# Optimization experiments

Hardware: AMD Instinct MI355X
Metric: run time of the kernel (lower is better)

Reference implementation:

```python
import jax, jax.numpy as jnp
import numpy as np

# Geometry (cone-beam circular trajectory, TIGRE-style ZYX volume layout)
NZ, NY, NX = 96, 96, 96          # geo.nVoxel
NV, NU = 96, 96                  # geo.nDetector (rows v, cols u)
N_ANGLES = 48
NS = 96                          # samples per ray (Joseph-style line integral)
DSO, DSD = 500.0, 1000.0         # source-origin / source-detector distances (mm)
DV = 1.0                         # voxel size (mm, isotropic)
DDET = 2.0                       # detector pixel size (mm)


def _trilinear(vol, pts):
    """Trilinear interpolation. vol: [B,Z,Y,X]; pts: [...,3] voxel coords (z,y,x).
    Points outside the volume contribute zero. Returns [B, ...]."""
    Z, Y, X = vol.shape[-3:]
    z, y, x = pts[..., 0], pts[..., 1], pts[..., 2]
    valid = ((z >= 0) & (z <= Z - 1) & (y >= 0) & (y <= Y - 1)
             & (x >= 0) & (x <= X - 1)).astype(vol.dtype)
    z = jnp.clip(z, 0.0, Z - 1.0)
    y = jnp.clip(y, 0.0, Y - 1.0)
    x = jnp.clip(x, 0.0, X - 1.0)
    z0 = jnp.minimum(jnp.floor(z).astype(jnp.int32), Z - 2)
    y0 = jnp.minimum(jnp.floor(y).astype(jnp.int32), Y - 2)
    x0 = jnp.minimum(jnp.floor(x).astype(jnp.int32), X - 2)
    fz = (z - z0).astype(vol.dtype)
    fy = (y - y0).astype(vol.dtype)
    fx = (x - x0).astype(vol.dtype)
    z1, y1, x1 = z0 + 1, y0 + 1, x0 + 1

    def g(zi, yi, xi):
        return vol[:, zi, yi, xi]  # [B, ...]

    out = (g(z0, y0, x0) * (1 - fz) * (1 - fy) * (1 - fx)
           + g(z0, y0, x1) * (1 - fz) * (1 - fy) * fx
           + g(z0, y1, x0) * (1 - fz) * fy * (1 - fx)
           + g(z0, y1, x1) * (1 - fz) * fy * fx
           + g(z1, y0, x0) * fz * (1 - fy) * (1 - fx)
           + g(z1, y0, x1) * fz * (1 - fy) * fx
           + g(z1, y1, x0) * fz * fy * (1 - fx)
           + g(z1, y1, x1) * fz * fy * fx)
    return out * valid


def _ray_points(theta):
    """Sample points (voxel coords, z,y,x order) along every detector ray for one angle.
    Returns pts [NV,NU,NS,3] and the integration step length (scalar)."""
    c, s = jnp.cos(theta), jnp.sin(theta)
    src = jnp.stack([DSO * c, DSO * s, jnp.float32(0.0)])            # world (x,y,z)
    det_c = jnp.stack([-(DSD - DSO) * c, -(DSD - DSO) * s, jnp.float32(0.0)])
    u_ax = jnp.stack([-s, c, jnp.float32(0.0)])
    v_ax = jnp.array([0.0, 0.0, 1.0], dtype=jnp.float32)
    u = (jnp.arange(NU, dtype=jnp.float32) - (NU - 1) / 2.0) * DDET
    v = (jnp.arange(NV, dtype=jnp.float32) - (NV - 1) / 2.0) * DDET
    pix = (det_c[None, None, :]
           + u[None, :, None] * u_ax[None, None, :]
           + v[:, None, None] * v_ax[None, None, :])                 # [NV,NU,3]
    d = pix - src[None, None, :]
    d = d / jnp.linalg.norm(d, axis=-1, keepdims=True)               # unit ray dirs
    # integrate over the volume bounding sphere around the isocenter
    R = 0.5 * np.sqrt((NX * DV) ** 2 + (NY * DV) ** 2 + (NZ * DV) ** 2)
    step = jnp.float32(2.0 * R / NS)
    t = jnp.float32(DSO - R) + (jnp.arange(NS, dtype=jnp.float32) + 0.5) * step
    pw = src[None, None, None, :] + d[:, :, None, :] * t[None, None, :, None]  # [NV,NU,NS,3] world xyz
    # world -> voxel index space, reorder to (z,y,x)
    iz = pw[..., 2] / DV + (NZ - 1) / 2.0
    iy = pw[..., 1] / DV + (NY - 1) / 2.0
    ix = pw[..., 0] / DV + (NX - 1) / 2.0
    return jnp.stack([iz, iy, ix], axis=-1), step


def _project(vol):
    """Cone-beam forward projection (tigre.Ax analogue). vol [B,NZ,NY,NX] -> sino [B,A,NV,NU]."""
    angles = jnp.linspace(0.0, 2.0 * np.pi, N_ANGLES, endpoint=False, dtype=jnp.float32)

    def body(_, theta):
        pts, step = _ray_points(theta)
        vals = _trilinear(vol, pts)          # [B,NV,NU,NS]
        return None, vals.sum(axis=-1) * step

    _, sino = jax.lax.scan(body, None, angles)   # [A,B,NV,NU]
    return jnp.transpose(sino, (1, 0, 2, 3))


def setup_inputs() -> dict:
    key = jax.random.key(0)
    x = jax.random.uniform(key, (2, NZ, NY, NX), dtype=jnp.float32)
    return {"x": x}


def reference(x):
    return _project(x)
```

## Files before the change

### kernel.cpp

```cpp
#include <hip/hip_runtime.h>
#include <math.h>


#define NZg 96
#define NYg 96
#define NXg 96
#define NVg 96
#define NUg 96
#define NAg 48
#define NSg 96
#define NBg 2
#define NVOX (NZg * NYg * NXg)
#define NRAY1 (NAg * NVg * NUg)
#define PLANE (NYg * NXg)

typedef float v4f __attribute__((ext_vector_type(4)));

__global__ __launch_bounds__(256) void pack_b2_dual_t(
    const float* __restrict__ vol, float2* __restrict__ qx,
    float2* __restrict__ qy) {
    __shared__ float2 tile[16][17];
    const int z      = blockIdx.x / 36;
    const int tileId = blockIdx.x % 36;
    const int y0 = (tileId / 6) * 16;
    const int x0 = (tileId % 6) * 16;
    const int tx = threadIdx.x & 15;
    const int ty = threadIdx.x >> 4;
    const int idx = (z * NYg + (y0 + ty)) * NXg + (x0 + tx);
    float2 p;
    p.x = vol[idx];
    p.y = vol[idx + NVOX];
    qx[idx] = p;
    tile[ty][tx] = p;
    __syncthreads();
    qy[(z * NXg + (x0 + ty)) * NYg + (y0 + tx)] = tile[tx][ty];
}

__global__ void make_trig(float2* __restrict__ trig) {
    const int a = threadIdx.x;
    if (a < NAg) {
        const float dtheta = 6.2831855f / 48.0f;
        const float theta  = (float)a * dtheta;
        float2 cs;
        cs.x = (float)cos((double)theta);
        cs.y = (float)sin((double)theta);
        trig[a] = cs;
    }
}

__device__ __forceinline__ void ray_setup_cs(
    int ridx, float c, float s, float& srcx, float& srcy,
    float& dx, float& dy, float& dz, int& k0, int& k1) {
#pragma clang fp contract(off)
    const int u   = ridx % NUg;
    int tmp       = ridx / NUg;
    const int v   = tmp % NVg;

    srcx = 500.0f * c;
    srcy = 500.0f * s;
    const float uu = ((float)u - 47.5f) * 2.0f;
    const float vv = ((float)v - 47.5f) * 2.0f;
    const float pixx = (-500.0f * c) + uu * (-s);
    const float pixy = (-500.0f * s) + uu * c;
    const float pixz = vv;

    const float dx0 = pixx - srcx;
    const float dy0 = pixy - srcy;
    const float dz0 = pixz;
    const float nrm = sqrtf((dx0 * dx0 + dy0 * dy0) + dz0 * dz0);
    dx = dx0 / nrm;
    dy = dy0 / nrm;
    dz = dz0 / nrm;

    const float stepf = (float)1.7320508075688773;
    const float t0f   = (float)416.8615612366939;

    const float LO = -47.51f, HI = 47.51f;
    float tlo = -1e30f, thi = 1e30f;
    {
        const float o3[3] = {srcx, srcy, 0.0f};
        const float d3[3] = {dx, dy, dz};
        bool empty = false;
        #pragma unroll
        for (int ax = 0; ax < 3; ++ax) {
            const float oo = o3[ax], dd = d3[ax];
            if (fabsf(dd) > 1e-8f) {
                const float inv = 1.0f / dd;
                const float ta = (LO - oo) * inv;
                const float tb = (HI - oo) * inv;
                tlo = fmaxf(tlo, fminf(ta, tb));
                thi = fminf(thi, fmaxf(ta, tb));
            } else if (oo < LO || oo > HI) {
                empty = true;
            }
        }
        if (empty) { tlo = 1.0f; thi = 0.0f; }
    }
    if (thi >= tlo) {
        k0 = (int)floorf((tlo - t0f) / stepf) - 2;
        k1 = (int)ceilf((thi - t0f) / stepf) + 2;
        k0 = max(k0, 0);
        k1 = min(k1, NSg - 1);
    } else {
        k0 = 1; k1 = 0;
    }
}

__global__ __launch_bounds__(256) void coneproj_b2dual_c2(
    const float2* __restrict__ qx, const float2* __restrict__ qy,
    const float2* __restrict__ trig, float* __restrict__ out) {
#pragma clang fp contract(off)
    const int lane     = threadIdx.x & 63;
    const int wid      = threadIdx.x >> 6;
    const int chunk    = wid >> 1;
    const int rayInBlk = ((wid & 1) << 6) + lane;
    const int ridx = blockIdx.x * 128 + rayInBlk;
    const int a    = ridx / (NUg * NVg);
    const float2 cs = trig[a];

    float srcx, srcy, dx, dy, dz;
    int k0, k1;
    ray_setup_cs(ridx, cs.x, cs.y, srcx, srcy, dx, dy, dz, k0, k1);

    const float stepf = (float)1.7320508075688773;
    const float t0f   = (float)416.8615612366939;

    const bool xfast = fabsf(cs.y) >= fabsf(cs.x);
    const float2* __restrict__ q = xfast ? qx : qy;
    const float src_i = xfast ? srcx : srcy;
    const float d_i   = xfast ? dx   : dy;
    const float src_m = xfast ? srcy : srcx;
    const float d_m   = xfast ? dy   : dx;

    const int len = (k1 - k0 + 2) >> 1;
    const int kb0 = k0 + chunk * len;
    const int kb1 = min(kb0 + len - 1, k1);

    float acc0 = 0.0f, acc1 = 0.0f;
    for (int k = kb0; k <= kb1; ++k) {
        const float tk = t0f + ((float)k + 0.5f) * stepf;
        const float ci = (src_i + d_i * tk) + 47.5f;
        const float cm = (src_m + d_m * tk) + 47.5f;
        const float iz = (dz * tk) + 47.5f;
        if (ci >= 0.0f && ci <= 95.0f &&
            cm >= 0.0f && cm <= 95.0f &&
            iz >= 0.0f && iz <= 95.0f) {
            const int i0 = min((int)ci, 94);
            const int m0 = min((int)cm, 94);
            const int z0 = min((int)iz, NZg - 2);
            const float fi = ci - (float)i0;
            const float fm = cm - (float)m0;
            const float fz = iz - (float)z0;
            const int base = (z0 * 96 + m0) * 96 + i0;
            const v4f r00 = *(const v4f*)(q + base);
            const v4f r01 = *(const v4f*)(q + base + 96);
            const v4f r10 = *(const v4f*)(q + base + PLANE);
            const v4f r11 = *(const v4f*)(q + base + PLANE + 96);
            {
                const float c00 = r00.x + fi * (r00.z - r00.x);
                const float c01 = r01.x + fi * (r01.z - r01.x);
                const float c10 = r10.x + fi * (r10.z - r10.x);
                const float c11 = r11.x + fi * (r11.z - r11.x);
                const float c0  = c00 + fm * (c01 - c00);
                const float c1  = c10 + fm * (c11 - c10);
                acc0 += c0 + fz * (c1 - c0);
            }
            {
                const float c00 = r00.y + fi * (r00.w - r00.y);
                const float c01 = r01.y + fi * (r01.w - r01.y);
                const float c10 = r10.y + fi * (r10.w - r10.y);
                const float c11 = r11.y + fi * (r11.w - r11.y);
                const float c0  = c00 + fm * (c01 - c00);
                const float c1  = c10 + fm * (c11 - c10);
                acc1 += c0 + fz * (c1 - c0);
            }
        }
    }

    __shared__ float p0[256];
    __shared__ float p1[256];
    p0[chunk * 128 + rayInBlk] = acc0;
    p1[chunk * 128 + rayInBlk] = acc1;
    __syncthreads();
    if (threadIdx.x < 128) {
        const int r = blockIdx.x * 128 + threadIdx.x;
        const float s0 = p0[threadIdx.x] + p0[threadIdx.x + 128];
        const float s1 = p1[threadIdx.x] + p1[threadIdx.x + 128];
        out[r]         = s0 * stepf;
        out[r + NRAY1] = s1 * stepf;
    }
}

__global__ __launch_bounds__(256) void pack_b2(
    const float* __restrict__ vol, float2* __restrict__ q) {
    const int i = blockIdx.x * blockDim.x + threadIdx.x;
    float2 p;
    p.x = vol[i];
    p.y = vol[i + NVOX];
    q[i] = p;
}

__device__ __forceinline__ void ray_setup(
    int ridx, float& srcx, float& srcy, float& dx, float& dy, float& dz,
    int& k0, int& k1) {
#pragma clang fp contract(off)
    const int a = ridx / (NUg * NVg);
    const float dtheta = 6.2831855f / 48.0f;
    const float theta  = (float)a * dtheta;
    const float c = (float)cos((double)theta);
    const float s = (float)sin((double)theta);
    ray_setup_cs(ridx, c, s, srcx, srcy, dx, dy, dz, k0, k1);
}

__global__ __launch_bounds__(256) void coneproj_b2x4(
    const float2* __restrict__ q, float* __restrict__ out) {
#pragma clang fp contract(off)
    const int ridx = blockIdx.x * blockDim.x + threadIdx.x;
    float srcx, srcy, dx, dy, dz;
    int k0, k1;
    ray_setup(ridx, srcx, srcy, dx, dy, dz, k0, k1);

    const float stepf = (float)1.7320508075688773;
    const float t0f   = (float)416.8615612366939;

    float acc0 = 0.0f, acc1 = 0.0f;
    for (int k = k0; k <= k1; ++k) {
        const float tk = t0f + ((float)k + 0.5f) * stepf;
        const float ix = (srcx + dx * tk) + 47.5f;
        const float iy = (srcy + dy * tk) + 47.5f;
        const float iz = (dz * tk) + 47.5f;
        if (ix >= 0.0f && ix <= 95.0f &&
            iy >= 0.0f && iy <= 95.0f &&
            iz >= 0.0f && iz <= 95.0f) {
            const int x0 = min((int)ix, NXg - 2);
            const int y0 = min((int)iy, NYg - 2);
            const int z0 = min((int)iz, NZg - 2);
            const float fx = ix - (float)x0;
            const float fy = iy - (float)y0;
            const float fz = iz - (float)z0;
            const int base = (z0 * NYg + y0) * NXg + x0;
            const v4f r00 = *(const v4f*)(q + base);
            const v4f r01 = *(const v4f*)(q + base + NXg);
            const v4f r10 = *(const v4f*)(q + base + PLANE);
            const v4f r11 = *(const v4f*)(q + base + PLANE + NXg);
            {
                const float c00 = r00.x + fx * (r00.z - r00.x);
                const float c01 = r01.x + fx * (r01.z - r01.x);
                const float c10 = r10.x + fx * (r10.z - r10.x);
                const float c11 = r11.x + fx * (r11.z - r11.x);
                const float c0  = c00 + fy * (c01 - c00);
                const float c1  = c10 + fy * (c11 - c10);
                acc0 += c0 + fz * (c1 - c0);
            }
            {
                const float c00 = r00.y + fx * (r00.w - r00.y);
                const float c01 = r01.y + fx * (r01.w - r01.y);
                const float c10 = r10.y + fx * (r10.w - r10.y);
                const float c11 = r11.y + fx * (r11.w - r11.y);
                const float c0  = c00 + fy * (c01 - c00);
                const float c1  = c10 + fy * (c11 - c10);
                acc1 += c0 + fz * (c1 - c0);
            }
        }
    }
    out[ridx]         = acc0 * stepf;
    out[ridx + NRAY1] = acc1 * stepf;
}

__global__ __launch_bounds__(256) void coneproj_direct(
    const float* __restrict__ vol, float* __restrict__ out) {
#pragma clang fp contract(off)
    const int gidx = blockIdx.x * blockDim.x + threadIdx.x;
    const int ridx = gidx % NRAY1;
    const int b    = gidx / NRAY1;
    float srcx, srcy, dx, dy, dz;
    int k0, k1;
    ray_setup(ridx, srcx, srcy, dx, dy, dz, k0, k1);

    const float stepf = (float)1.7320508075688773;
    const float t0f   = (float)416.8615612366939;

    const float* __restrict__ volb = vol + (size_t)b * NVOX;

    float acc = 0.0f;
    for (int k = k0; k <= k1; ++k) {
        const float tk = t0f + ((float)k + 0.5f) * stepf;
        const float ix = (srcx + dx * tk) + 47.5f;
        const float iy = (srcy + dy * tk) + 47.5f;
        const float iz = (dz * tk) + 47.5f;
        if (ix >= 0.0f && ix <= 95.0f &&
            iy >= 0.0f && iy <= 95.0f &&
            iz >= 0.0f && iz <= 95.0f) {
            const int x0 = min((int)ix, NXg - 2);
            const int y0 = min((int)iy, NYg - 2);
            const int z0 = min((int)iz, NZg - 2);
            const float fx = ix - (float)x0;
            const float fy = iy - (float)y0;
            const float fz = iz - (float)z0;
            const float* p = volb + ((z0 * NYg + y0) * NXg + x0);
            const float v000 = p[0];
            const float v001 = p[1];
            const float v010 = p[NXg];
            const float v011 = p[NXg + 1];
            const float v100 = p[NYg * NXg];
            const float v101 = p[NYg * NXg + 1];
            const float v110 = p[NYg * NXg + NXg];
            const float v111 = p[NYg * NXg + NXg + 1];
            const float c00 = v000 + fx * (v001 - v000);
            const float c01 = v010 + fx * (v011 - v010);
            const float c10 = v100 + fx * (v101 - v100);
            const float c11 = v110 + fx * (v111 - v110);
            const float c0  = c00 + fy * (c01 - c00);
            const float c1  = c10 + fy * (c11 - c10);
            acc += c0 + fz * (c1 - c0);
        }
    }
    out[gidx] = acc * stepf;
}

extern "C" void kernel_launch(void* const* d_in, const int* in_sizes, int n_in,
                              void* d_out, int out_size, void* d_ws, size_t ws_size,
                              hipStream_t stream) {
    const float* vol = (const float*)d_in[0];
    float* out = (float*)d_out;
    const size_t need_dual   = 2 * (size_t)NVOX * sizeof(float2)
                             + (size_t)NAg * sizeof(float2);
    const size_t need_single = (size_t)NVOX * sizeof(float2);
    if (ws_size >= need_dual) {
        float2* qx   = (float2*)d_ws;
        float2* qy   = qx + NVOX;
        float2* trig = qy + NVOX;
        pack_b2_dual_t<<<96 * 36, 256, 0, stream>>>(vol, qx, qy);
        make_trig<<<1, 64, 0, stream>>>(trig);
        coneproj_b2dual_c2<<<NRAY1 / 128, 256, 0, stream>>>(qx, qy, trig, out);
    } else if (ws_size >= need_single) {
        float2* q = (float2*)d_ws;
        pack_b2<<<NVOX / 256, 256, 0, stream>>>(vol, q);
        coneproj_b2x4<<<NRAY1 / 256, 256, 0, stream>>>(q, out);
    } else {
        coneproj_direct<<<(NBg * NRAY1) / 256, 256, 0, stream>>>(vol, out);
    }
}
```

Baseline: 190.3 us.

## Fuse volume packing and projection into one cooperative kernel with grid sync

Merges the dual-layout pack kernel and the projection kernel into a single cooperative launch of 1728 blocks. The blocks first pack the volume tiles, then synchronise across the grid and project one ray per thread. The intent is to remove a kernel launch boundary and its gap. It also drops the earlier split of each ray's samples across two waves with a shared-memory reduction, so each thread now walks the whole ray. This gives less parallelism per ray, and a 1728-block cooperative launch may fail residency checks, in which case it falls back to two kernels.

After: 397.4 us. +108.8%, slower.

```diff
diff --git a/kernel.cpp b/kernel.cpp
--- a/kernel.cpp
+++ b/kernel.cpp
@@ -1,5 +1,8 @@
 #include <hip/hip_runtime.h>
+#include <hip/hip_cooperative_groups.h>
 #include <math.h>
+
+namespace cg = cooperative_groups;
 
 
 #define NZg 96
@@ -13,28 +16,9 @@
 #define NVOX (NZg * NYg * NXg)
 #define NRAY1 (NAg * NVg * NUg)
 #define PLANE (NYg * NXg)
+#define NBLK 1728
 
 typedef float v4f __attribute__((ext_vector_type(4)));
-
-__global__ __launch_bounds__(256) void pack_b2_dual_t(
-    const float* __restrict__ vol, float2* __restrict__ qx,
-    float2* __restrict__ qy) {
-    __shared__ float2 tile[16][17];
-    const int z      = blockIdx.x / 36;
-    const int tileId = blockIdx.x % 36;
-    const int y0 = (tileId / 6) * 16;
-    const int x0 = (tileId % 6) * 16;
-    const int tx = threadIdx.x & 15;
-    const int ty = threadIdx.x >> 4;
-    const int idx = (z * NYg + (y0 + ty)) * NXg + (x0 + tx);
-    float2 p;
-    p.x = vol[idx];
-    p.y = vol[idx + NVOX];
-    qx[idx] = p;
-    tile[ty][tx] = p;
-    __syncthreads();
-    qy[(z * NXg + (x0 + ty)) * NYg + (y0 + tx)] = tile[tx][ty];
-}
 
 __global__ void make_trig(float2* __restrict__ trig) {
     const int a = threadIdx.x;
@@ -106,18 +90,10 @@
     }
 }
 
-__global__ __launch_bounds__(256) void coneproj_b2dual_c2(
-    const float2* __restrict__ qx, const float2* __restrict__ qy,
-    const float2* __restrict__ trig, float* __restrict__ out) {
+__device__ __forceinline__ void project_ray(
+    int ridx, float2 cs, const float2* __restrict__ qx,
+    const float2* __restrict__ qy, float* __restrict__ out) {
 #pragma clang fp contract(off)
-    const int lane     = threadIdx.x & 63;
-    const int wid      = threadIdx.x >> 6;
-    const int chunk    = wid >> 1;
-    const int rayInBlk = ((wid & 1) << 6) + lane;
-    const int ridx = blockIdx.x * 128 + rayInBlk;
-    const int a    = ridx / (NUg * NVg);
-    const float2 cs = trig[a];
-
     float srcx, srcy, dx, dy, dz;
     int k0, k1;
     ray_setup_cs(ridx, cs.x, cs.y, srcx, srcy, dx, dy, dz, k0, k1);
@@ -132,12 +108,8 @@
     const float src_m = xfast ? srcy : srcx;
     const float d_m   = xfast ? dy   : dx;
 
-    const int len = (k1 - k0 + 2) >> 1;
-    const int kb0 = k0 + chunk * len;
-    const int kb1 = min(kb0 + len - 1, k1);
-
     float acc0 = 0.0f, acc1 = 0.0f;
-    for (int k = kb0; k <= kb1; ++k) {
+    for (int k = k0; k <= k1; ++k) {
         const float tk = t0f + ((float)k + 0.5f) * stepf;
         const float ci = (src_i + d_i * tk) + 47.5f;
         const float cm = (src_m + d_m * tk) + 47.5f;
@@ -176,28 +148,67 @@
             }
         }
     }
-
-    __shared__ float p0[256];
-    __shared__ float p1[256];
-    p0[chunk * 128 + rayInBlk] = acc0;
-    p1[chunk * 128 + rayInBlk] = acc1;
+    out[ridx]         = acc0 * stepf;
+    out[ridx + NRAY1] = acc1 * stepf;
+}
+
+__global__ __launch_bounds__(256) void coneproj_fused(
+    const float* __restrict__ vol, float2* __restrict__ qx,
+    float2* __restrict__ qy, const float2* __restrict__ trig,
+    float* __restrict__ out) {
+    __shared__ float2 tile[16][17];
+
+    const int tx = threadIdx.x & 15;
+    const int ty = threadIdx.x >> 4;
+    for (int pb = blockIdx.x; pb < 96 * 36; pb += NBLK) {
+        const int z      = pb / 36;
+        const int tileId = pb % 36;
+        const int y0 = (tileId / 6) * 16;
+        const int x0 = (tileId % 6) * 16;
+        const int idx = (z * NYg + (y0 + ty)) * NXg + (x0 + tx);
+        float2 p;
+        p.x = vol[idx];
+        p.y = vol[idx + NVOX];
+        qx[idx] = p;
+        __syncthreads();
+        tile[ty][tx] = p;
+        __syncthreads();
+        qy[(z * NXg + (x0 + ty)) * NYg + (y0 + tx)] = tile[tx][ty];
+    }
+
+    cg::this_grid().sync();
+
+    const int ridx = blockIdx.x * 256 + threadIdx.x;
+    const int a    = ridx / (NUg * NVg);
+    project_ray(ridx, trig[a], qx, qy, out);
+}
+
+__global__ __launch_bounds__(256) void pack_b2_dual_t(
+    const float* __restrict__ vol, float2* __restrict__ qx,
+    float2* __restrict__ qy) {
+    __shared__ float2 tile[16][17];
+    const int z      = blockIdx.x / 36;
+    const int tileId = blockIdx.x % 36;
+    const int y0 = (tileId / 6) * 16;
+    const int x0 = (tileId % 6) * 16;
+    const int tx = threadIdx.x & 15;
+    const int ty = threadIdx.x >> 4;
+    const int idx = (z * NYg + (y0 + ty)) * NXg + (x0 + tx);
+    float2 p;
+    p.x = vol[idx];
+    p.y = vol[idx + NVOX];
+    qx[idx] = p;
+    tile[ty][tx] = p;
     __syncthreads();
-    if (threadIdx.x < 128) {
-        const int r = blockIdx.x * 128 + threadIdx.x;
-        const float s0 = p0[threadIdx.x] + p0[threadIdx.x + 128];
-        const float s1 = p1[threadIdx.x] + p1[threadIdx.x + 128];
-        out[r]         = s0 * stepf;
-        out[r + NRAY1] = s1 * stepf;
-    }
-}
-
-__global__ __launch_bounds__(256) void pack_b2(
-    const float* __restrict__ vol, float2* __restrict__ q) {
-    const int i = blockIdx.x * blockDim.x + threadIdx.x;
-    float2 p;
-    p.x = vol[i];
-    p.y = vol[i + NVOX];
-    q[i] = p;
+    qy[(z * NXg + (x0 + ty)) * NYg + (y0 + tx)] = tile[tx][ty];
+}
+
+__global__ __launch_bounds__(256) void coneproj_b2dual(
+    const float2* __restrict__ qx, const float2* __restrict__ qy,
+    const float2* __restrict__ trig, float* __restrict__ out) {
+    const int ridx = blockIdx.x * blockDim.x + threadIdx.x;
+    const int a    = ridx / (NUg * NVg);
+    project_ray(ridx, trig[a], qx, qy, out);
 }
 
 __device__ __forceinline__ void ray_setup(
@@ -210,61 +221,6 @@
     const float c = (float)cos((double)theta);
     const float s = (float)sin((double)theta);
     ray_setup_cs(ridx, c, s, srcx, srcy, dx, dy, dz, k0, k1);
-}
-
-__global__ __launch_bounds__(256) void coneproj_b2x4(
-    const float2* __restrict__ q, float* __restrict__ out) {
-#pragma clang fp contract(off)
-    const int ridx = blockIdx.x * blockDim.x + threadIdx.x;
-    float srcx, srcy, dx, dy, dz;
-    int k0, k1;
-    ray_setup(ridx, srcx, srcy, dx, dy, dz, k0, k1);
-
-    const float stepf = (float)1.7320508075688773;
-    const float t0f   = (float)416.8615612366939;
-
-    float acc0 = 0.0f, acc1 = 0.0f;
-    for (int k = k0; k <= k1; ++k) {
-        const float tk = t0f + ((float)k + 0.5f) * stepf;
-        const float ix = (srcx + dx * tk) + 47.5f;
-        const float iy = (srcy + dy * tk) + 47.5f;
-        const float iz = (dz * tk) + 47.5f;
-        if (ix >= 0.0f && ix <= 95.0f &&
-            iy >= 0.0f && iy <= 95.0f &&
-            iz >= 0.0f && iz <= 95.0f) {
-            const int x0 = min((int)ix, NXg - 2);
-            const int y0 = min((int)iy, NYg - 2);
-            const int z0 = min((int)iz, NZg - 2);
-            const float fx = ix - (float)x0;
-            const float fy = iy - (float)y0;
-            const float fz = iz - (float)z0;
-            const int base = (z0 * NYg + y0) * NXg + x0;
-            const v4f r00 = *(const v4f*)(q + base);
-            const v4f r01 = *(const v4f*)(q + base + NXg);
-            const v4f r10 = *(const v4f*)(q + base + PLANE);
-            const v4f r11 = *(const v4f*)(q + base + PLANE + NXg);
-            {
-                const float c00 = r00.x + fx * (r00.z - r00.x);
-                const float c01 = r01.x + fx * (r01.z - r01.x);
-                const float c10 = r10.x + fx * (r10.z - r10.x);
-                const float c11 = r11.x + fx * (r11.z - r11.x);
-                const float c0  = c00 + fy * (c01 - c00);
-                const float c1  = c10 + fy * (c11 - c10);
-                acc0 += c0 + fz * (c1 - c0);
-            }
-            {
-                const float c00 = r00.y + fx * (r00.w - r00.y);
-                const float c01 = r01.y + fx * (r01.w - r01.y);
-                const float c10 = r10.y + fx * (r10.w - r10.y);
-                const float c11 = r11.y + fx * (r11.w - r11.y);
-                const float c0  = c00 + fy * (c01 - c00);
-                const float c1  = c10 + fy * (c11 - c10);
-                acc1 += c0 + fz * (c1 - c0);
-            }
-        }
-    }
-    out[ridx]         = acc0 * stepf;
-    out[ridx + NRAY1] = acc1 * stepf;
 }
 
 __global__ __launch_bounds__(256) void coneproj_direct(
@@ -330,13 +286,17 @@
         float2* qx   = (float2*)d_ws;
         float2* qy   = qx + NVOX;
         float2* trig = qy + NVOX;
-        pack_b2_dual_t<<<96 * 36, 256, 0, stream>>>(vol, qx, qy);
         make_trig<<<1, 64, 0, stream>>>(trig);
-        coneproj_b2dual_c2<<<NRAY1 / 128, 256, 0, stream>>>(qx, qy, trig, out);
+        void* args[] = {(void*)&vol, (void*)&qx, (void*)&qy,
+                        (void*)&trig, (void*)&out};
+        hipError_t e = hipLaunchCooperativeKernel(
+            (void*)coneproj_fused, dim3(NBLK), dim3(256), args, 0, stream);
+        if (e != hipSuccess) {
+            pack_b2_dual_t<<<96 * 36, 256, 0, stream>>>(vol, qx, qy);
+            coneproj_b2dual<<<NRAY1 / 256, 256, 0, stream>>>(qx, qy, trig, out);
+        }
     } else if (ws_size >= need_single) {
-        float2* q = (float2*)d_ws;
-        pack_b2<<<NVOX / 256, 256, 0, stream>>>(vol, q);
-        coneproj_b2x4<<<NRAY1 / 256, 256, 0, stream>>>(q, out);
+        coneproj_direct<<<(NBg * NRAY1) / 256, 256, 0, stream>>>(vol, out);
     } else {
         coneproj_direct<<<(NBg * NRAY1) / 256, 256, 0, stream>>>(vol, out);
     }
```

## Pack volume z-fastest with both z-neighbours per voxel, map threads v-fastest

Applied to the files above, without the earlier changes.

Adds a z-fastest packed layout where each entry holds both batches at z and z+1, so each sample's trilinear lookup becomes four 16-byte loads along x/y neighbours. Threads are ordered with detector row v fastest, so adjacent lanes step mostly along z and land on nearby memory. The trig table is built inside the pack kernel, which removes one launch, and the two-chunk split of each ray with its shared-memory reduction is dropped. The cost is a workspace twice as large, output writes that are no longer coalesced (stride NU), and rays that are no longer split, which lowers parallelism.

Result: faster. 173.7 us (-8.7%).

```diff
diff --git a/kernel.cpp b/kernel.cpp
--- a/kernel.cpp
+++ b/kernel.cpp
@@ -15,6 +15,156 @@
 #define PLANE (NYg * NXg)
 
 typedef float v4f __attribute__((ext_vector_type(4)));
+
+__global__ __launch_bounds__(256) void pack_b2_zfast(
+    const float* __restrict__ vol, v4f* __restrict__ D,
+    float2* __restrict__ trig) {
+    const int j = blockIdx.x * 256 + threadIdx.x;
+    const int z = j % NZg;
+    const int t = j / NZg;
+    const int x = t % NXg;
+    const int y = t / NXg;
+    const int rd = (z * NYg + y) * NXg + x;
+    const float b0 = vol[rd];
+    const float b1 = vol[rd + NVOX];
+    const float b0n = (z < 95) ? vol[rd + NYg * NXg] : 0.0f;
+    const float b1n = (z < 95) ? vol[rd + NYg * NXg + NVOX] : 0.0f;
+    v4f e; e.x = b0; e.y = b1; e.z = b0n; e.w = b1n;
+    D[j] = e;
+    if (j < NAg) {
+        const float dtheta = 6.2831855f / 48.0f;
+        const float theta  = (float)j * dtheta;
+        float2 cs;
+        cs.x = (float)cos((double)theta);
+        cs.y = (float)sin((double)theta);
+        trig[j] = cs;
+    }
+}
+
+__device__ __forceinline__ void ray_setup_uv(
+    int u, int v, float c, float s, float& srcx, float& srcy,
+    float& dx, float& dy, float& dz, int& k0, int& k1) {
+#pragma clang fp contract(off)
+    srcx = 500.0f * c;
+    srcy = 500.0f * s;
+    const float uu = ((float)u - 47.5f) * 2.0f;
+    const float vv = ((float)v - 47.5f) * 2.0f;
+    const float pixx = (-500.0f * c) + uu * (-s);
+    const float pixy = (-500.0f * s) + uu * c;
+    const float pixz = vv;
+
+    const float dx0 = pixx - srcx;
+    const float dy0 = pixy - srcy;
+    const float dz0 = pixz;
+    const float nrm = sqrtf((dx0 * dx0 + dy0 * dy0) + dz0 * dz0);
+    dx = dx0 / nrm;
+    dy = dy0 / nrm;
+    dz = dz0 / nrm;
+
+    const float stepf = (float)1.7320508075688773;
+    const float t0f   = (float)416.8615612366939;
+
+    const float LO = -47.51f, HI = 47.51f;
+    float tlo = -1e30f, thi = 1e30f;
+    {
+        const float o3[3] = {srcx, srcy, 0.0f};
+        const float d3[3] = {dx, dy, dz};
+        bool empty = false;
+        #pragma unroll
+        for (int ax = 0; ax < 3; ++ax) {
+            const float oo = o3[ax], dd = d3[ax];
+            if (fabsf(dd) > 1e-8f) {
+                const float inv = 1.0f / dd;
+                const float ta = (LO - oo) * inv;
+                const float tb = (HI - oo) * inv;
+                tlo = fmaxf(tlo, fminf(ta, tb));
+                thi = fminf(thi, fmaxf(ta, tb));
+            } else if (oo < LO || oo > HI) {
+                empty = true;
+            }
+        }
+        if (empty) { tlo = 1.0f; thi = 0.0f; }
+    }
+    if (thi >= tlo) {
+        k0 = (int)floorf((tlo - t0f) / stepf) - 2;
+        k1 = (int)ceilf((thi - t0f) / stepf) + 2;
+        k0 = max(k0, 0);
+        k1 = min(k1, NSg - 1);
+    } else {
+        k0 = 1; k1 = 0;
+    }
+}
+
+__global__ __launch_bounds__(256) void coneproj_zfast(
+    const v4f* __restrict__ D, const float2* __restrict__ trig,
+    float* __restrict__ out) {
+#pragma clang fp contract(off)
+    const int idx = blockIdx.x * 256 + threadIdx.x;
+    const int v   = idx % NVg;
+    int tmp       = idx / NVg;
+    const int u   = tmp % NUg;
+    const int a   = tmp / NUg;
+    const float2 cs = trig[a];
+
+    float srcx, srcy, dx, dy, dz;
+    int k0, k1;
+    ray_setup_uv(u, v, cs.x, cs.y, srcx, srcy, dx, dy, dz, k0, k1);
+
+    const float stepf = (float)1.7320508075688773;
+    const float t0f   = (float)416.8615612366939;
+
+    float acc0 = 0.0f, acc1 = 0.0f;
+    for (int k = k0; k <= k1; ++k) {
+        const float tk = t0f + ((float)k + 0.5f) * stepf;
+        const float ix = (srcx + dx * tk) + 47.5f;
+        const float iy = (srcy + dy * tk) + 47.5f;
+        const float iz = (dz * tk) + 47.5f;
+        if (ix >= 0.0f && ix <= 95.0f &&
+            iy >= 0.0f && iy <= 95.0f &&
+            iz >= 0.0f && iz <= 95.0f) {
+            const int x0 = min((int)ix, NXg - 2);
+            const int y0 = min((int)iy, NYg - 2);
+            const int z0 = min((int)iz, NZg - 2);
+            const float fx = ix - (float)x0;
+            const float fy = iy - (float)y0;
+            const float fz = iz - (float)z0;
+            const int base = (y0 * NXg + x0) * NZg + z0;
+            const v4f r00 = D[base];
+            const v4f r01 = D[base + NZg];
+            const v4f r10 = D[base + NXg * NZg];
+            const v4f r11 = D[base + NXg * NZg + NZg];
+            {
+                const float w00 = r00.x + fz * (r00.z - r00.x);
+                const float w01 = r01.x + fz * (r01.z - r01.x);
+                const float w10 = r10.x + fz * (r10.z - r10.x);
+                const float w11 = r11.x + fz * (r11.z - r11.x);
+                const float e0  = w00 + fx * (w01 - w00);
+                const float e1  = w10 + fx * (w11 - w10);
+                acc0 += e0 + fy * (e1 - e0);
+            }
+            {
+                const float w00 = r00.y + fz * (r00.w - r00.y);
+                const float w01 = r01.y + fz * (r01.w - r01.y);
+                const float w10 = r10.y + fz * (r10.w - r10.y);
+                const float w11 = r11.y + fz * (r11.w - r11.y);
+                const float e0  = w00 + fx * (w01 - w00);
+                const float e1  = w10 + fx * (w11 - w10);
+                acc1 += e0 + fy * (e1 - e0);
+            }
+        }
+    }
+    const int oidx = (a * NVg + v) * NUg + u;
+    out[oidx]         = acc0 * stepf;
+    out[oidx + NRAY1] = acc1 * stepf;
+}
+
+__device__ __forceinline__ void ray_setup_cs(
+    int ridx, float c, float s, float& srcx, float& srcy,
+    float& dx, float& dy, float& dz, int& k0, int& k1) {
+    const int u = ridx % NUg;
+    const int v = (ridx / NUg) % NVg;
+    ray_setup_uv(u, v, c, s, srcx, srcy, dx, dy, dz, k0, k1);
+}
 
 __global__ __launch_bounds__(256) void pack_b2_dual_t(
     const float* __restrict__ vol, float2* __restrict__ qx,
@@ -48,76 +198,13 @@
     }
 }
 
-__device__ __forceinline__ void ray_setup_cs(
-    int ridx, float c, float s, float& srcx, float& srcy,
-    float& dx, float& dy, float& dz, int& k0, int& k1) {
-#pragma clang fp contract(off)
-    const int u   = ridx % NUg;
-    int tmp       = ridx / NUg;
-    const int v   = tmp % NVg;
-
-    srcx = 500.0f * c;
-    srcy = 500.0f * s;
-    const float uu = ((float)u - 47.5f) * 2.0f;
-    const float vv = ((float)v - 47.5f) * 2.0f;
-    const float pixx = (-500.0f * c) + uu * (-s);
-    const float pixy = (-500.0f * s) + uu * c;
-    const float pixz = vv;
-
-    const float dx0 = pixx - srcx;
-    const float dy0 = pixy - srcy;
-    const float dz0 = pixz;
-    const float nrm = sqrtf((dx0 * dx0 + dy0 * dy0) + dz0 * dz0);
-    dx = dx0 / nrm;
-    dy = dy0 / nrm;
-    dz = dz0 / nrm;
-
-    const float stepf = (float)1.7320508075688773;
-    const float t0f   = (float)416.8615612366939;
-
-    const float LO = -47.51f, HI = 47.51f;
-    float tlo = -1e30f, thi = 1e30f;
-    {
-        const float o3[3] = {srcx, srcy, 0.0f};
-        const float d3[3] = {dx, dy, dz};
-        bool empty = false;
-        #pragma unroll
-        for (int ax = 0; ax < 3; ++ax) {
-            const float oo = o3[ax], dd = d3[ax];
-            if (fabsf(dd) > 1e-8f) {
-                const float inv = 1.0f / dd;
-                const float ta = (LO - oo) * inv;
-                const float tb = (HI - oo) * inv;
-                tlo = fmaxf(tlo, fminf(ta, tb));
-                thi = fminf(thi, fmaxf(ta, tb));
-            } else if (oo < LO || oo > HI) {
-                empty = true;
-            }
-        }
-        if (empty) { tlo = 1.0f; thi = 0.0f; }
-    }
-    if (thi >= tlo) {
-        k0 = (int)floorf((tlo - t0f) / stepf) - 2;
-        k1 = (int)ceilf((thi - t0f) / stepf) + 2;
-        k0 = max(k0, 0);
-        k1 = min(k1, NSg - 1);
-    } else {
-        k0 = 1; k1 = 0;
-    }
-}
-
-__global__ __launch_bounds__(256) void coneproj_b2dual_c2(
+__global__ __launch_bounds__(256) void coneproj_b2dual(
     const float2* __restrict__ qx, const float2* __restrict__ qy,
     const float2* __restrict__ trig, float* __restrict__ out) {
 #pragma clang fp contract(off)
-    const int lane     = threadIdx.x & 63;
-    const int wid      = threadIdx.x >> 6;
-    const int chunk    = wid >> 1;
-    const int rayInBlk = ((wid & 1) << 6) + lane;
-    const int ridx = blockIdx.x * 128 + rayInBlk;
+    const int ridx = blockIdx.x * blockDim.x + threadIdx.x;
     const int a    = ridx / (NUg * NVg);
     const float2 cs = trig[a];
-
     float srcx, srcy, dx, dy, dz;
     int k0, k1;
     ray_setup_cs(ridx, cs.x, cs.y, srcx, srcy, dx, dy, dz, k0, k1);
@@ -132,12 +219,8 @@
     const float src_m = xfast ? srcy : srcx;
     const float d_m   = xfast ? dy   : dx;
 
-    const int len = (k1 - k0 + 2) >> 1;
-    const int kb0 = k0 + chunk * len;
-    const int kb1 = min(kb0 + len - 1, k1);
-
     float acc0 = 0.0f, acc1 = 0.0f;
-    for (int k = kb0; k <= kb1; ++k) {
+    for (int k = k0; k <= k1; ++k) {
         const float tk = t0f + ((float)k + 0.5f) * stepf;
         const float ci = (src_i + d_i * tk) + 47.5f;
         const float cm = (src_m + d_m * tk) + 47.5f;
@@ -176,93 +259,6 @@
             }
         }
     }
-
-    __shared__ float p0[256];
-    __shared__ float p1[256];
-    p0[chunk * 128 + rayInBlk] = acc0;
-    p1[chunk * 128 + rayInBlk] = acc1;
-    __syncthreads();
-    if (threadIdx.x < 128) {
-        const int r = blockIdx.x * 128 + threadIdx.x;
-        const float s0 = p0[threadIdx.x] + p0[threadIdx.x + 128];
-        const float s1 = p1[threadIdx.x] + p1[threadIdx.x + 128];
-        out[r]         = s0 * stepf;
-        out[r + NRAY1] = s1 * stepf;
-    }
-}
-
-__global__ __launch_bounds__(256) void pack_b2(
-    const float* __restrict__ vol, float2* __restrict__ q) {
-    const int i = blockIdx.x * blockDim.x + threadIdx.x;
-    float2 p;
-    p.x = vol[i];
-    p.y = vol[i + NVOX];
-    q[i] = p;
-}
-
-__device__ __forceinline__ void ray_setup(
-    int ridx, float& srcx, float& srcy, float& dx, float& dy, float& dz,
-    int& k0, int& k1) {
-#pragma clang fp contract(off)
-    const int a = ridx / (NUg * NVg);
-    const float dtheta = 6.2831855f / 48.0f;
-    const float theta  = (float)a * dtheta;
-    const float c = (float)cos((double)theta);
-    const float s = (float)sin((double)theta);
-    ray_setup_cs(ridx, c, s, srcx, srcy, dx, dy, dz, k0, k1);
-}
-
-__global__ __launch_bounds__(256) void coneproj_b2x4(
-    const float2* __restrict__ q, float* __restrict__ out) {
-#pragma clang fp contract(off)
-    const int ridx = blockIdx.x * blockDim.x + threadIdx.x;
-    float srcx, srcy, dx, dy, dz;
-    int k0, k1;
-    ray_setup(ridx, srcx, srcy, dx, dy, dz, k0, k1);
-
-    const float stepf = (float)1.7320508075688773;
-    const float t0f   = (float)416.8615612366939;
-
-    float acc0 = 0.0f, acc1 = 0.0f;
-    for (int k = k0; k <= k1; ++k) {
-        const float tk = t0f + ((float)k + 0.5f) * stepf;
-        const float ix = (srcx + dx * tk) + 47.5f;
-        const float iy = (srcy + dy * tk) + 47.5f;
-        const float iz = (dz * tk) + 47.5f;
-        if (ix >= 0.0f && ix <= 95.0f &&
-            iy >= 0.0f && iy <= 95.0f &&
-            iz >= 0.0f && iz <= 95.0f) {
-            const int x0 = min((int)ix, NXg - 2);
-            const int y0 = min((int)iy, NYg - 2);
-            const int z0 = min((int)iz, NZg - 2);
-            const float fx = ix - (float)x0;
-            const float fy = iy - (float)y0;
-            const float fz = iz - (float)z0;
-            const int base = (z0 * NYg + y0) * NXg + x0;
-            const v4f r00 = *(const v4f*)(q + base);
-            const v4f r01 = *(const v4f*)(q + base + NXg);
-            const v4f r10 = *(const v4f*)(q + base + PLANE);
-            const v4f r11 = *(const v4f*)(q + base + PLANE + NXg);
-            {
-                const float c00 = r00.x + fx * (r00.z - r00.x);
-                const float c01 = r01.x + fx * (r01.z - r01.x);
-                const float c10 = r10.x + fx * (r10.z - r10.x);
-                const float c11 = r11.x + fx * (r11.z - r11.x);
-                const float c0  = c00 + fy * (c01 - c00);
-                const float c1  = c10 + fy * (c11 - c10);
-                acc0 += c0 + fz * (c1 - c0);
-            }
-            {
-                const float c00 = r00.y + fx * (r00.w - r00.y);
-                const float c01 = r01.y + fx * (r01.w - r01.y);
-                const float c10 = r10.y + fx * (r10.w - r10.y);
-                const float c11 = r11.y + fx * (r11.w - r11.y);
-                const float c0  = c00 + fy * (c01 - c00);
-                const float c1  = c10 + fy * (c11 - c10);
-                acc1 += c0 + fz * (c1 - c0);
-            }
-        }
-    }
     out[ridx]         = acc0 * stepf;
     out[ridx + NRAY1] = acc1 * stepf;
 }
@@ -273,9 +269,14 @@
     const int gidx = blockIdx.x * blockDim.x + threadIdx.x;
     const int ridx = gidx % NRAY1;
     const int b    = gidx / NRAY1;
+    const int a = ridx / (NUg * NVg);
+    const float dtheta = 6.2831855f / 48.0f;
+    const float theta  = (float)a * dtheta;
+    const float c = (float)cos((double)theta);
+    const float s = (float)sin((double)theta);
     float srcx, srcy, dx, dy, dz;
     int k0, k1;
-    ray_setup(ridx, srcx, srcy, dx, dy, dz, k0, k1);
+    ray_setup_cs(ridx, c, s, srcx, srcy, dx, dy, dz, k0, k1);
 
     const float stepf = (float)1.7320508075688773;
     const float t0f   = (float)416.8615612366939;
@@ -323,20 +324,22 @@
                               hipStream_t stream) {
     const float* vol = (const float*)d_in[0];
     float* out = (float*)d_out;
-    const size_t need_dual   = 2 * (size_t)NVOX * sizeof(float2)
-                             + (size_t)NAg * sizeof(float2);
-    const size_t need_single = (size_t)NVOX * sizeof(float2);
-    if (ws_size >= need_dual) {
+    const size_t need_zf   = (size_t)NVOX * sizeof(v4f)
+                           + (size_t)NAg * sizeof(float2);
+    const size_t need_dual = 2 * (size_t)NVOX * sizeof(float2)
+                           + (size_t)NAg * sizeof(float2);
+    if (ws_size >= need_zf) {
+        v4f*    D    = (v4f*)d_ws;
+        float2* trig = (float2*)(D + NVOX);
+        pack_b2_zfast<<<NVOX / 256, 256, 0, stream>>>(vol, D, trig);
+        coneproj_zfast<<<NRAY1 / 256, 256, 0, stream>>>(D, trig, out);
+    } else if (ws_size >= need_dual) {
         float2* qx   = (float2*)d_ws;
         float2* qy   = qx + NVOX;
         float2* trig = qy + NVOX;
         pack_b2_dual_t<<<96 * 36, 256, 0, stream>>>(vol, qx, qy);
         make_trig<<<1, 64, 0, stream>>>(trig);
-        coneproj_b2dual_c2<<<NRAY1 / 128, 256, 0, stream>>>(qx, qy, trig, out);
-    } else if (ws_size >= need_single) {
-        float2* q = (float2*)d_ws;
-        pack_b2<<<NVOX / 256, 256, 0, stream>>>(vol, q);
-        coneproj_b2x4<<<NRAY1 / 256, 256, 0, stream>>>(q, out);
+        coneproj_b2dual<<<NRAY1 / 256, 256, 0, stream>>>(qx, qy, trig, out);
     } else {
         coneproj_direct<<<(NBg * NRAY1) / 256, 256, 0, stream>>>(vol, out);
     }
```
